# Optimization experiments

Hardware: AMD Instinct MI355X
Metric: run time of the kernel (lower is better)

Reference implementation:

```python
import jax, jax.numpy as jnp
import numpy as np


def _dF(field, c):
    """Central differences of component c of field [B,X,Y,Z,C] -> [B,X-2,Y-2,Z-2,3]."""
    f = field[..., c]
    dx = (f[:, 2:, 1:-1, 1:-1] - f[:, :-2, 1:-1, 1:-1]) * 0.5
    dy = (f[:, 1:-1, 2:, 1:-1] - f[:, 1:-1, :-2, 1:-1]) * 0.5
    dz = (f[:, 1:-1, 1:-1, 2:] - f[:, 1:-1, 1:-1, :-2]) * 0.5
    return jnp.stack((dx, dy, dz), axis=4)


def setup_inputs() -> dict:
    key = jax.random.key(0)
    grid = jax.random.normal(key, (2, 160, 160, 160, 3), dtype=jnp.float32)
    return {"grid": grid}


def reference(grid):
    # First derivatives of each displacement component: [B,X-2,Y-2,Z-2,3]
    dx = _dF(grid, 0)
    dy = _dF(grid, 1)
    dz = _dF(grid, 2)
    # Second derivatives: [B,X-4,Y-4,Z-4,3]
    dxx = _dF(dx, 0)
    dyy = _dF(dy, 1)
    dzz = _dF(dz, 2)
    dxy = _dF(dx, 1)
    dyz = _dF(dy, 2)
    dxz = _dF(dx, 2)
    penalty = jnp.sum(dxx ** 2 + dyy ** 2 + dzz ** 2
                      + 2.0 * (dxy ** 2 + dyz ** 2 + dxz ** 2))
    return penalty / dxx.size
```

## Files before the change

kernel.cpp:

```cpp
#include <hip/hip_runtime.h>

#define OY 480
#define OX 76800
#define SB 12288000
#define JT 4
#define NROW 8
#define IT 12
#define NSEG 13
#define SLICEF 3840
#define CTHR 156
#define NBLK 1014
#define INV_SIZE (1.0f/22778496.0f)

__device__ __forceinline__ float4 ld4p(const float* p){ return *reinterpret_cast<const float4*>(p); }
__device__ __forceinline__ void st4p(float* p, float4 v){ *reinterpret_cast<float4*>(p) = v; }

__device__ __forceinline__ void ld24(float* d, const float* p){
    float4 x0=ld4p(p), x1=ld4p(p+4), x2=ld4p(p+8), x3=ld4p(p+12), x4=ld4p(p+16), x5=ld4p(p+20);
    d[0]=x0.x; d[1]=x0.y; d[2]=x0.z; d[3]=x0.w;
    d[4]=x1.x; d[5]=x1.y; d[6]=x1.z; d[7]=x1.w;
    d[8]=x2.x; d[9]=x2.y; d[10]=x2.z; d[11]=x2.w;
    d[12]=x3.x; d[13]=x3.y; d[14]=x3.z; d[15]=x3.w;
    d[16]=x4.x; d[17]=x4.y; d[18]=x4.z; d[19]=x4.w;
    d[20]=x5.x; d[21]=x5.y; d[22]=x5.z; d[23]=x5.w;
}
__device__ __forceinline__ void ld16(float* d, const float* p){
    float4 x0=ld4p(p), x1=ld4p(p+4), x2=ld4p(p+8), x3=ld4p(p+12);
    d[0]=x0.x; d[1]=x0.y; d[2]=x0.z; d[3]=x0.w;
    d[4]=x1.x; d[5]=x1.y; d[6]=x1.z; d[7]=x1.w;
    d[8]=x2.x; d[9]=x2.y; d[10]=x2.z; d[11]=x2.w;
    d[12]=x3.x; d[13]=x3.y; d[14]=x3.z; d[15]=x3.w;
}

#define STEP(P, V0a, V0b, DP) { \
    const int s = 2*d + (P); \
    const bool doLoad = (s <= 14); \
    float4 a0, a1, a2, a3; \
    if (doLoad) { \
        const float* bp = G + (size_t)(i0 - 1 + s) * OX; \
        a0 = ld4p(bp+gof0); a1 = ld4p(bp+gof1); a2 = ld4p(bp+gof2); \
        if (tl) a3 = ld4p(bp+gof3); \
    } \
    if (act) { \
        const bool doWS = (s >= 2) && (s <= 13); \
        const bool doXY = (s >= 3) && (s <= 14); \
        const bool doXX = (s >= 4); \
        const float* Lr = lds + (P)*SLICEF + oj; \
        float fcn[24]; ld24(fcn, Lr); \
        float v0c[4], dzc0[4], dzc1[4], dzc2[4]; \
        _Pragma("unroll") for (int v=0; v<4; ++v) { \
            v0c[v]  = fcn[6+3*v]; \
            dzc0[v] = fcn[9+3*v]  - fcn[3+3*v]; \
            dzc1[v] = fcn[10+3*v] - fcn[4+3*v]; \
            dzc2[v] = fcn[11+3*v] - fcn[5+3*v]; \
        } \
        if (doWS) { \
            _Pragma("unroll") for (int v=0; v<4; ++v) { \
                float h0 = fcn[12+3*v] - 2.f*fcn[6+3*v] + fcn[3*v];   cls2 = fmaf(h0,h0,cls2); \
                float h1 = fcn[13+3*v] - 2.f*fcn[7+3*v] + fcn[1+3*v]; cls2 = fmaf(h1,h1,cls2); \
                float h2 = fcn[14+3*v] - 2.f*fcn[8+3*v] + fcn[2+3*v]; cls1 = fmaf(h2,h2,cls1); \
            } \
            float p2[16], m2[16]; \
            ld16(p2, Lr + 2*OY + 4); \
            ld16(m2, Lr - 2*OY + 4); \
            _Pragma("unroll") for (int v=0; v<4; ++v) { \
                float h0 = p2[2+3*v] - 2.f*fcn[6+3*v] + m2[2+3*v]; cls2 = fmaf(h0,h0,cls2); \
                float h1 = p2[3+3*v] - 2.f*fcn[7+3*v] + m2[3+3*v]; cls1 = fmaf(h1,h1,cls1); \
            } \
        } \
        float fp[24], fm[24]; \
        ld24(fp, Lr + OY); ld24(fm, Lr - OY); \
        float dyc0[4], dyc1[4]; \
        _Pragma("unroll") for (int v=0; v<4; ++v) { \
            dyc0[v] = fp[3*(v+2)]   - fm[3*(v+2)]; \
            dyc1[v] = fp[3*(v+2)+1] - fm[3*(v+2)+1]; \
        } \
        if (doWS) { \
            _Pragma("unroll") for (int v=0; v<4; ++v) { \
                float ha = (fp[3*(v+3)]   - fm[3*(v+3)])   - (fp[3*(v+1)]   - fm[3*(v+1)]);   cls4 = fmaf(ha,ha,cls4); \
                float hb = (fp[3*(v+3)+1] - fm[3*(v+3)+1]) - (fp[3*(v+1)+1] - fm[3*(v+1)+1]); cls3 = fmaf(hb,hb,cls3); \
                float hc = (fp[3*(v+3)+2] - fm[3*(v+3)+2]) - (fp[3*(v+1)+2] - fm[3*(v+1)+2]); cls1 = fmaf(hc,hc,cls1); \
            } \
        } \
        _Pragma("unroll") for (int v=0; v<4; ++v) { \
            if (doXY) { float h; \
                h = dyc0[v] - DP[0][v]; cls3 = fmaf(h,h,cls3); \
                h = dyc1[v] - DP[1][v]; cls1 = fmaf(h,h,cls1); \
                h = dzc0[v] - DP[2][v]; cls3 = fmaf(h,h,cls3); \
                h = dzc1[v] - DP[3][v]; cls2 = fmaf(h,h,cls2); \
                h = dzc2[v] - DP[4][v]; cls1 = fmaf(h,h,cls1); \
            } \
            DP[0][v] = dyc0[v]; DP[1][v] = dyc1[v]; \
            DP[2][v] = dzc0[v]; DP[3][v] = dzc1[v]; DP[4][v] = dzc2[v]; \
            float w2v = V0a[v], w4v = V0b[v]; \
            if (doXX) { float h = v0c[v] - 2.f*w2v + w4v; cls1 = fmaf(h,h,cls1); } \
            V0b[v] = w2v; V0a[v] = v0c[v]; \
        } \
    } \
    if (doLoad) { \
        float* Lw = lds + ((P)^1)*SLICEF; \
        st4p(Lw+lof0, a0); st4p(Lw+lof1, a1); st4p(Lw+lof2, a2); \
        if (tl) st4p(Lw+lof3, a3); \
    } \
    __syncthreads(); \
}

__global__ __launch_bounds__(256, 3)
void be_partials(const float* __restrict__ g, float* __restrict__ partial) {
    __shared__ float lds[2*SLICEF];
    __shared__ float wsum[4];

    const int tid = threadIdx.x;
    const int bid = blockIdx.x;
    const int is = bid % NSEG;
    int r1 = bid / NSEG;
    const int jt = r1 % 39;
    const int bb = r1 / 39;

    const int j0 = 2 + jt*JT;
    const int i0 = 2 + is*IT;
    const float* __restrict__ G = g + (size_t)bb*SB + (size_t)(j0-2)*OY;

    const bool tl = tid < 192;
    const int gof0 = 4*tid,        lof0 = gof0;
    const int gof1 = 4*(tid+256),  lof1 = gof1;
    const int gof2 = 4*(tid+512),  lof2 = gof2;
    const int gof3 = 4*(tid+768),  lof3 = gof3;

    const bool act = tid < CTHR;
    int cj = tid / 39, cq = tid - (tid/39)*39;
    if (!act) { cj = 0; cq = 0; }
    const int oj = (cj+2)*OY + 12*cq;

    float v0A0[4], v0A1[4], v0B0[4], v0B1[4];
    float dpA[5][4], dpB[5][4];
    #pragma unroll
    for (int v=0; v<4; ++v) {
        v0A0[v]=v0A1[v]=v0B0[v]=v0B1[v]=0.f;
        #pragma unroll
        for (int q=0; q<5; ++q) { dpA[q][v]=0.f; dpB[q][v]=0.f; }
    }
    float cls1=0.f, cls2=0.f, cls3=0.f, cls4=0.f;

    {
        const float* bp = G + (size_t)(i0-2)*OX;
        float4 a0=ld4p(bp+gof0), a1=ld4p(bp+gof1), a2=ld4p(bp+gof2);
        st4p(lds+lof0, a0); st4p(lds+lof1, a1); st4p(lds+lof2, a2);
        if (tl) { float4 a3=ld4p(bp+gof3); st4p(lds+lof3, a3); }
    }
    __syncthreads();

    #pragma unroll 1
    for (int d = 0; d < 8; ++d) {
        STEP(0, v0A0, v0A1, dpA)
        STEP(1, v0B0, v0B1, dpB)
    }

    float sv = fmaf(2.f, cls2, cls1);
    sv = fmaf(3.f, cls3, sv);
    sv = fmaf(4.f, cls4, sv);
    sv *= 0.0625f;

    #pragma unroll
    for (int off = 32; off > 0; off >>= 1) sv += __shfl_down(sv, off, 64);
    if ((tid & 63) == 0) wsum[tid >> 6] = sv;
    __syncthreads();
    if (tid == 0)
        partial[bid] = (wsum[0] + wsum[1]) + (wsum[2] + wsum[3]);
}

__global__ __launch_bounds__(256)
void be_final(const float* __restrict__ partial, float* __restrict__ out) {
    float s = 0.0f;
    for (int i = threadIdx.x; i < NBLK; i += 256) s += partial[i];
    #pragma unroll
    for (int off = 32; off > 0; off >>= 1) s += __shfl_down(s, off, 64);
    __shared__ float ws[4];
    if ((threadIdx.x & 63) == 0) ws[threadIdx.x >> 6] = s;
    __syncthreads();
    if (threadIdx.x == 0)
        out[0] = ((ws[0] + ws[1]) + (ws[2] + ws[3])) * INV_SIZE;
}

extern "C" void kernel_launch(void* const* d_in, const int* in_sizes, int n_in,
                              void* d_out, int out_size, void* d_ws, size_t ws_size,
                              hipStream_t stream) {
    const float* grid = (const float*)d_in[0];
    float* out = (float*)d_out;
    float* partials = (float*)d_ws;

    be_partials<<<dim3(NBLK), dim3(256), 0, stream>>>(grid, partials);
    be_final<<<1, 256, 0, stream>>>(partials, out);
}
```

Before: 164.1 us.

## Remap threads so y-neighbours sit in DPP rows and use row shifts for y-stencils

```diff
diff --git a/kernel.cpp b/kernel.cpp
--- a/kernel.cpp
+++ b/kernel.cpp
@@ -3,14 +3,23 @@
 #define OY 480
 #define OX 76800
 #define SB 12288000
-#define JT 4
-#define NROW 8
+#define RST 212
+#define SLICEF (16*RST)
 #define IT 12
 #define NSEG 13
-#define SLICEF 3840
-#define CTHR 156
 #define NBLK 1014
 #define INV_SIZE (1.0f/22778496.0f)
+
+#define ROW_SHL1 0x101
+#define ROW_SHL2 0x102
+#define ROW_SHR1 0x111
+#define ROW_SHR2 0x112
+
+template<int CTRL>
+__device__ __forceinline__ float dppf(float x){
+    return __int_as_float(__builtin_amdgcn_update_dpp(
+        0, __float_as_int(x), CTRL, 0xF, 0xF, true));
+}
 
 __device__ __forceinline__ float4 ld4p(const float* p){ return *reinterpret_cast<const float4*>(p); }
 __device__ __forceinline__ void st4p(float* p, float4 v){ *reinterpret_cast<float4*>(p) = v; }
@@ -24,13 +33,6 @@
     d[16]=x4.x; d[17]=x4.y; d[18]=x4.z; d[19]=x4.w;
     d[20]=x5.x; d[21]=x5.y; d[22]=x5.z; d[23]=x5.w;
 }
-__device__ __forceinline__ void ld16(float* d, const float* p){
-    float4 x0=ld4p(p), x1=ld4p(p+4), x2=ld4p(p+8), x3=ld4p(p+12);
-    d[0]=x0.x; d[1]=x0.y; d[2]=x0.z; d[3]=x0.w;
-    d[4]=x1.x; d[5]=x1.y; d[6]=x1.z; d[7]=x1.w;
-    d[8]=x2.x; d[9]=x2.y; d[10]=x2.z; d[11]=x2.w;
-    d[12]=x3.x; d[13]=x3.y; d[14]=x3.z; d[15]=x3.w;
-}
 
 #define STEP(P, V0a, V0b, DP) { \
     const int s = 2*d + (P); \
@@ -38,74 +40,65 @@
     float4 a0, a1, a2, a3; \
     if (doLoad) { \
         const float* bp = G + (size_t)(i0 - 1 + s) * OX; \
-        a0 = ld4p(bp+gof0); a1 = ld4p(bp+gof1); a2 = ld4p(bp+gof2); \
-        if (tl) a3 = ld4p(bp+gof3); \
+        a0 = ld4p(bp+gof0); a1 = ld4p(bp+gof1); a2 = ld4p(bp+gof2); a3 = ld4p(bp+gof3); \
     } \
-    if (act) { \
-        const bool doWS = (s >= 2) && (s <= 13); \
-        const bool doXY = (s >= 3) && (s <= 14); \
-        const bool doXX = (s >= 4); \
+    if (qact) { \
         const float* Lr = lds + (P)*SLICEF + oj; \
-        float fcn[24]; ld24(fcn, Lr); \
-        float v0c[4], dzc0[4], dzc1[4], dzc2[4]; \
+        float x[24]; ld24(x, Lr); \
+        float dz0[4], dz1[4], dz2[4], dy0[4], dy1[4], v0c[4]; \
         _Pragma("unroll") for (int v=0; v<4; ++v) { \
-            v0c[v]  = fcn[6+3*v]; \
-            dzc0[v] = fcn[9+3*v]  - fcn[3+3*v]; \
-            dzc1[v] = fcn[10+3*v] - fcn[4+3*v]; \
-            dzc2[v] = fcn[11+3*v] - fcn[5+3*v]; \
+            v0c[v] = x[3*v+6]; \
+            dz0[v] = x[3*v+9]  - x[3*v+3]; \
+            dz1[v] = x[3*v+10] - x[3*v+4]; \
+            dz2[v] = x[3*v+11] - x[3*v+5]; \
+            dy0[v] = dppf<ROW_SHR1>(x[3*v+6]) - dppf<ROW_SHL1>(x[3*v+6]); \
+            dy1[v] = dppf<ROW_SHR1>(x[3*v+7]) - dppf<ROW_SHL1>(x[3*v+7]); \
         } \
-        if (doWS) { \
+        if (s >= 2 && s <= 13) { \
             _Pragma("unroll") for (int v=0; v<4; ++v) { \
-                float h0 = fcn[12+3*v] - 2.f*fcn[6+3*v] + fcn[3*v];   cls2 = fmaf(h0,h0,cls2); \
-                float h1 = fcn[13+3*v] - 2.f*fcn[7+3*v] + fcn[1+3*v]; cls2 = fmaf(h1,h1,cls2); \
-                float h2 = fcn[14+3*v] - 2.f*fcn[8+3*v] + fcn[2+3*v]; cls1 = fmaf(h2,h2,cls1); \
-            } \
-            float p2[16], m2[16]; \
-            ld16(p2, Lr + 2*OY + 4); \
-            ld16(m2, Lr - 2*OY + 4); \
-            _Pragma("unroll") for (int v=0; v<4; ++v) { \
-                float h0 = p2[2+3*v] - 2.f*fcn[6+3*v] + m2[2+3*v]; cls2 = fmaf(h0,h0,cls2); \
-                float h1 = p2[3+3*v] - 2.f*fcn[7+3*v] + m2[3+3*v]; cls1 = fmaf(h1,h1,cls1); \
+                float c0 = x[3*v+6], c1 = x[3*v+7]; \
+                float hy0 = dppf<ROW_SHR2>(c0) - 2.f*c0 + dppf<ROW_SHL2>(c0); \
+                float hy1 = dppf<ROW_SHR2>(c1) - 2.f*c1 + dppf<ROW_SHL2>(c1); \
+                float yz0 = dppf<ROW_SHR1>(dz0[v]) - dppf<ROW_SHL1>(dz0[v]); \
+                float yz1 = dppf<ROW_SHR1>(dz1[v]) - dppf<ROW_SHL1>(dz1[v]); \
+                float yz2 = dppf<ROW_SHR1>(dz2[v]) - dppf<ROW_SHL1>(dz2[v]); \
+                if (vr) { \
+                    float zz0 = x[3*v+12] - 2.f*x[3*v+6] + x[3*v]; \
+                    float zz1 = x[3*v+13] - 2.f*x[3*v+7] + x[3*v+1]; \
+                    float zz2 = x[3*v+14] - 2.f*x[3*v+8] + x[3*v+2]; \
+                    cls2 = fmaf(zz0,zz0,cls2); cls2 = fmaf(zz1,zz1,cls2); cls1 = fmaf(zz2,zz2,cls1); \
+                    cls2 = fmaf(hy0,hy0,cls2); cls1 = fmaf(hy1,hy1,cls1); \
+                    cls4 = fmaf(yz0,yz0,cls4); cls3 = fmaf(yz1,yz1,cls3); cls1 = fmaf(yz2,yz2,cls1); \
+                } \
             } \
         } \
-        float fp[24], fm[24]; \
-        ld24(fp, Lr + OY); ld24(fm, Lr - OY); \
-        float dyc0[4], dyc1[4]; \
+        const bool eXY = vr && (s >= 3) && (s <= 14); \
+        const bool eXX = vr && (s >= 4); \
         _Pragma("unroll") for (int v=0; v<4; ++v) { \
-            dyc0[v] = fp[3*(v+2)]   - fm[3*(v+2)]; \
-            dyc1[v] = fp[3*(v+2)+1] - fm[3*(v+2)+1]; \
-        } \
-        if (doWS) { \
-            _Pragma("unroll") for (int v=0; v<4; ++v) { \
-                float ha = (fp[3*(v+3)]   - fm[3*(v+3)])   - (fp[3*(v+1)]   - fm[3*(v+1)]);   cls4 = fmaf(ha,ha,cls4); \
-                float hb = (fp[3*(v+3)+1] - fm[3*(v+3)+1]) - (fp[3*(v+1)+1] - fm[3*(v+1)+1]); cls3 = fmaf(hb,hb,cls3); \
-                float hc = (fp[3*(v+3)+2] - fm[3*(v+3)+2]) - (fp[3*(v+1)+2] - fm[3*(v+1)+2]); cls1 = fmaf(hc,hc,cls1); \
+            if (eXY) { float h; \
+                h = dy0[v] - DP[0][v]; cls3 = fmaf(h,h,cls3); \
+                h = dy1[v] - DP[1][v]; cls1 = fmaf(h,h,cls1); \
+                h = dz0[v] - DP[2][v]; cls3 = fmaf(h,h,cls3); \
+                h = dz1[v] - DP[3][v]; cls2 = fmaf(h,h,cls2); \
+                h = dz2[v] - DP[4][v]; cls1 = fmaf(h,h,cls1); \
             } \
-        } \
-        _Pragma("unroll") for (int v=0; v<4; ++v) { \
-            if (doXY) { float h; \
-                h = dyc0[v] - DP[0][v]; cls3 = fmaf(h,h,cls3); \
-                h = dyc1[v] - DP[1][v]; cls1 = fmaf(h,h,cls1); \
-                h = dzc0[v] - DP[2][v]; cls3 = fmaf(h,h,cls3); \
-                h = dzc1[v] - DP[3][v]; cls2 = fmaf(h,h,cls2); \
-                h = dzc2[v] - DP[4][v]; cls1 = fmaf(h,h,cls1); \
-            } \
-            DP[0][v] = dyc0[v]; DP[1][v] = dyc1[v]; \
-            DP[2][v] = dzc0[v]; DP[3][v] = dzc1[v]; DP[4][v] = dzc2[v]; \
-            float w2v = V0a[v], w4v = V0b[v]; \
-            if (doXX) { float h = v0c[v] - 2.f*w2v + w4v; cls1 = fmaf(h,h,cls1); } \
-            V0b[v] = w2v; V0a[v] = v0c[v]; \
+            DP[0][v] = dy0[v]; DP[1][v] = dy1[v]; \
+            DP[2][v] = dz0[v]; DP[3][v] = dz1[v]; DP[4][v] = dz2[v]; \
+            if (eXX) { float h = v0c[v] - 2.f*V0a[v] + V0b[v]; cls1 = fmaf(h,h,cls1); } \
+            V0b[v] = V0a[v]; V0a[v] = v0c[v]; \
         } \
     } \
     if (doLoad) { \
         float* Lw = lds + ((P)^1)*SLICEF; \
-        st4p(Lw+lof0, a0); st4p(Lw+lof1, a1); st4p(Lw+lof2, a2); \
-        if (tl) st4p(Lw+lof3, a3); \
+        if (wv0) st4p(Lw+lof0, a0); \
+        if (wv1) st4p(Lw+lof1, a1); \
+        if (wv2) st4p(Lw+lof2, a2); \
+        if (wv3) st4p(Lw+lof3, a3); \
     } \
     __syncthreads(); \
 }
 
-__global__ __launch_bounds__(256, 3)
+__global__ __launch_bounds__(256)
 void be_partials(const float* __restrict__ g, float* __restrict__ partial) {
     __shared__ float lds[2*SLICEF];
     __shared__ float wsum[4];
@@ -114,23 +107,39 @@
     const int bid = blockIdx.x;
     const int is = bid % NSEG;
     int r1 = bid / NSEG;
-    const int jt = r1 % 39;
-    const int bb = r1 / 39;
-
-    const int j0 = 2 + jt*JT;
-    const int i0 = 2 + is*IT;
-    const float* __restrict__ G = g + (size_t)bb*SB + (size_t)(j0-2)*OY;
-
-    const bool tl = tid < 192;
-    const int gof0 = 4*tid,        lof0 = gof0;
-    const int gof1 = 4*(tid+256),  lof1 = gof1;
-    const int gof2 = 4*(tid+512),  lof2 = gof2;
-    const int gof3 = 4*(tid+768),  lof3 = gof3;
-
-    const bool act = tid < CTHR;
-    int cj = tid / 39, cq = tid - (tid/39)*39;
-    if (!act) { cj = 0; cq = 0; }
-    const int oj = (cj+2)*OY + 12*cq;
+    const int zt = r1 % 3;  r1 /= 3;
+    const int jt = r1 % 13;
+    const int bb = r1 / 13;
+
+    const int j0  = 2 + jt*12;
+    const int zlo = 64*zt;
+    const int i0  = 2 + is*IT;
+    const float* __restrict__ G = g + (size_t)bb*SB + (size_t)(j0-2)*OY + 3*zlo;
+
+    const int vmaxq0 = (480 - 3*zlo) >> 2;
+    const int vmaxq = vmaxq0 < 51 ? vmaxq0 : 51;
+    int gof0,gof1,gof2,gof3, lof0,lof1,lof2,lof3;
+    bool wv0,wv1,wv2,wv3;
+    {
+        int f, row, pos, vp;
+        f = tid;       row = f/53; pos = f - 53*row; vp = pos < vmaxq ? pos : vmaxq-1;
+        gof0 = row*OY + 4*vp; lof0 = row*RST + 4*pos; wv0 = pos < vmaxq;
+        f = tid + 256; row = f/53; pos = f - 53*row; vp = pos < vmaxq ? pos : vmaxq-1;
+        gof1 = row*OY + 4*vp; lof1 = row*RST + 4*pos; wv1 = pos < vmaxq;
+        f = tid + 512; row = f/53; pos = f - 53*row; vp = pos < vmaxq ? pos : vmaxq-1;
+        gof2 = row*OY + 4*vp; lof2 = row*RST + 4*pos; wv2 = pos < vmaxq;
+        if (tid < 80) {
+            f = tid + 768; row = f/53; pos = f - 53*row; vp = pos < vmaxq ? pos : vmaxq-1;
+            gof3 = row*OY + 4*vp; lof3 = row*RST + 4*pos; wv3 = pos < vmaxq;
+        } else { gof3 = 0; lof3 = 0; wv3 = false; }
+    }
+
+    const int r = tid & 15;
+    const int Q = tid >> 4;
+    const int qmax = (zt == 2) ? 7 : 16;
+    const bool qact = Q < qmax;
+    const bool vr = (r >= 2) && (r <= 13);
+    const int oj = r*RST + 12*Q;
 
     float v0A0[4], v0A1[4], v0B0[4], v0B1[4];
     float dpA[5][4], dpB[5][4];
@@ -144,9 +153,11 @@
 
     {
         const float* bp = G + (size_t)(i0-2)*OX;
-        float4 a0=ld4p(bp+gof0), a1=ld4p(bp+gof1), a2=ld4p(bp+gof2);
-        st4p(lds+lof0, a0); st4p(lds+lof1, a1); st4p(lds+lof2, a2);
-        if (tl) { float4 a3=ld4p(bp+gof3); st4p(lds+lof3, a3); }
+        float4 a0=ld4p(bp+gof0), a1=ld4p(bp+gof1), a2=ld4p(bp+gof2), a3=ld4p(bp+gof3);
+        if (wv0) st4p(lds+lof0, a0);
+        if (wv1) st4p(lds+lof1, a1);
+        if (wv2) st4p(lds+lof2, a2);
+        if (wv3) st4p(lds+lof3, a3);
     }
     __syncthreads();
 
```

Result: faster. 152.4 us (-7.1%).
